# Optimization experiments

Hardware: AMD Instinct MI355X
Metric: run time of the kernel (lower is better)

The kernel has to match this reference:

```python
import jax, jax.numpy as jnp
import numpy as np

_PADDING_NUM = -1


def setup_inputs() -> dict:
    key = jax.random.key(0)
    B, M, S, C = 4096, 64, 64, 4096  # batch, num_buckets, multiplex_count, channels
    x = jax.random.normal(key, (B, C), dtype=jnp.float32)
    # Full packing: each slot holds a unique object index (no padding).
    assignments = jnp.arange(B, dtype=jnp.int32).reshape(M, S)
    return {"x": x, "assignments": assignments}


def reference(x, assignments):
    """Mux (dispatch) then demux (combine) via precomputed one-hot transition matrices.

    x:           (B, C)  data-space tensor
    assignments: (M, S)  object index per (bucket, slot); _PADDING_NUM (-1) -> zero slot
    returns demuxed (B, C): data-space tensor recovered from multiplex space.
    """
    B = x.shape[0]
    valid = (assignments >= 0)  # (M, S)
    # Transition matrix: (M, S, B); padding slots map to all-zero rows.
    T = jax.nn.one_hot(jnp.where(valid, assignments, 0), B, dtype=x.dtype)
    T = T * valid[..., None].astype(x.dtype)
    # mux: place each valid object into its (bucket, slot); padding slots are zeros.
    muxed = jnp.einsum('msb,bc->msc', T, x)  # (M, S, C)
    # demux: gather slots back to data space in object-index order.
    demuxed = jnp.einsum('msb,msc->bc', T, muxed)  # (B, C)
    return demuxed
```

## Files before the change

kernel.cpp:

```cpp
#include <hip/hip_runtime.h>


__global__ void mux_count_kernel(const int* __restrict__ assignments, int ms,
                                 int* __restrict__ count) {
    int i = blockIdx.x * blockDim.x + threadIdx.x;
    if (i < ms) {
        int a = assignments[i];
        if (a >= 0) atomicAdd(&count[a], 1);
    }
}

__global__ void mux_scale_kernel(const float4* __restrict__ x,
                                 const int* __restrict__ count,
                                 float4* __restrict__ out, int c_vec) {
    int b = blockIdx.y;
    int j = blockIdx.x * blockDim.x + threadIdx.x;
    if (j < c_vec) {
        float s = (float)count[b];
        long i = (long)b * c_vec + j;
        float4 v = x[i];
        v.x *= s; v.y *= s; v.z *= s; v.w *= s;
        out[i] = v;
    }
}

extern "C" void kernel_launch(void* const* d_in, const int* in_sizes, int n_in,
                              void* d_out, int out_size, void* d_ws, size_t ws_size,
                              hipStream_t stream) {
    const float* x = (const float*)d_in[0];
    const int* assignments = (const int*)d_in[1];
    float* out = (float*)d_out;

    const int B = 4096;
    const int C = 4096;
    const int ms = in_sizes[1];
    const int c_vec = C / 4;

    int* count = (int*)d_ws;

    hipMemsetAsync(count, 0, (size_t)B * sizeof(int), stream);

    {
        dim3 block(256);
        dim3 grid((ms + 255) / 256);
        mux_count_kernel<<<grid, block, 0, stream>>>(assignments, ms, count);
    }

    {
        dim3 block(256);
        dim3 grid((c_vec + 255) / 256, B);
        mux_scale_kernel<<<grid, block, 0, stream>>>((const float4*)x, count,
                                                     (float4*)out, c_vec);
    }
}
```

Before: 114.3 us.

## Fuse count and scale into one kernel with per-block redundant counting

Replaces the memset, the atomic histogram kernel and the scale kernel with a single kernel. Each block handles one row, recounts how often its row index appears in the assignments by scanning all 4096 entries with a wave shuffle and shared-memory reduction, then scales the row. This drops two launches and the atomic traffic. In exchange every block rereads the 16KB assignment array, though it should stay in cache, and sizes are hardcoded.

```diff
diff --git a/kernel.cpp b/kernel.cpp
--- a/kernel.cpp
+++ b/kernel.cpp
@@ -1,26 +1,51 @@
 #include <hip/hip_runtime.h>
 
 
-__global__ void mux_count_kernel(const int* __restrict__ assignments, int ms,
-                                 int* __restrict__ count) {
-    int i = blockIdx.x * blockDim.x + threadIdx.x;
-    if (i < ms) {
-        int a = assignments[i];
-        if (a >= 0) atomicAdd(&count[a], 1);
+#define BLOCK 256
+#define C_VEC 1024
+#define VPT 4
+#define MS_VEC 1024
+#define APT 4
+
+__global__ __launch_bounds__(BLOCK) void mux_fused_kernel(
+    const float4* __restrict__ x,
+    const int4* __restrict__ a4,
+    float4* __restrict__ out) {
+    const int b = blockIdx.x;
+    const int tid = threadIdx.x;
+
+    const long base = (long)b * C_VEC;
+    float4 v[VPT];
+#pragma unroll
+    for (int k = 0; k < VPT; ++k)
+        v[k] = x[base + tid + BLOCK * k];
+
+    int local = 0;
+#pragma unroll
+    for (int k = 0; k < APT; ++k) {
+        int4 a = a4[tid + BLOCK * k];
+        local += (a.x == b) + (a.y == b) + (a.z == b) + (a.w == b);
     }
-}
 
-__global__ void mux_scale_kernel(const float4* __restrict__ x,
-                                 const int* __restrict__ count,
-                                 float4* __restrict__ out, int c_vec) {
-    int b = blockIdx.y;
-    int j = blockIdx.x * blockDim.x + threadIdx.x;
-    if (j < c_vec) {
-        float s = (float)count[b];
-        long i = (long)b * c_vec + j;
-        float4 v = x[i];
-        v.x *= s; v.y *= s; v.z *= s; v.w *= s;
-        out[i] = v;
+#pragma unroll
+    for (int off = 32; off > 0; off >>= 1)
+        local += __shfl_down(local, off, 64);
+
+    __shared__ int wave_sum[BLOCK / 64];
+    __shared__ float s_scale;
+    const int wave = tid >> 6;
+    if ((tid & 63) == 0) wave_sum[wave] = local;
+    __syncthreads();
+    if (tid == 0)
+        s_scale = (float)(wave_sum[0] + wave_sum[1] + wave_sum[2] + wave_sum[3]);
+    __syncthreads();
+    const float s = s_scale;
+
+#pragma unroll
+    for (int k = 0; k < VPT; ++k) {
+        float4 w = v[k];
+        w.x *= s; w.y *= s; w.z *= s; w.w *= s;
+        out[base + tid + BLOCK * k] = w;
     }
 }
 
@@ -32,24 +57,6 @@
     float* out = (float*)d_out;
 
     const int B = 4096;
-    const int C = 4096;
-    const int ms = in_sizes[1];
-    const int c_vec = C / 4;
-
-    int* count = (int*)d_ws;
-
-    hipMemsetAsync(count, 0, (size_t)B * sizeof(int), stream);
-
-    {
-        dim3 block(256);
-        dim3 grid((ms + 255) / 256);
-        mux_count_kernel<<<grid, block, 0, stream>>>(assignments, ms, count);
-    }
-
-    {
-        dim3 block(256);
-        dim3 grid((c_vec + 255) / 256, B);
-        mux_scale_kernel<<<grid, block, 0, stream>>>((const float4*)x, count,
-                                                     (float4*)out, c_vec);
-    }
+    mux_fused_kernel<<<dim3(B), dim3(BLOCK), 0, stream>>>(
+        (const float4*)x, (const int4*)assignments, (float4*)out);
 }
```

Result: no change. 112.1 us (-1.9%).
